# Kernel optimization log

Measured on AMD Instinct MI355X. Metric: run time of the kernel, lower is better.

Reference implementation:

```python
import jax, jax.numpy as jnp
import numpy as np

NUM_EXPERTS = 16
TOP_K = 4
N_GROUP = 4
TOPK_GROUP = 2
SCALING = 2.5


def setup_inputs() -> dict:
    key = jax.random.key(0)
    ks = jax.random.split(key, 9)
    B, S, H, I = 2, 1024, 2048, 1024
    w = lambda k, shape: jax.random.normal(k, shape, jnp.float32) * 0.02
    return {
        "hidden_states": jax.random.normal(ks[0], (B, S, H), jnp.float32),
        "gate_weight": w(ks[1], (NUM_EXPERTS, H)),
        "expert_bias": jnp.zeros((NUM_EXPERTS,), jnp.float32),
        "gate_proj": w(ks[2], (NUM_EXPERTS, I, H)),
        "up_proj": w(ks[3], (NUM_EXPERTS, I, H)),
        "down_proj": w(ks[4], (NUM_EXPERTS, H, I)),
        "shared_gate": w(ks[5], (I, H)),
        "shared_up": w(ks[6], (I, H)),
        "shared_down": w(ks[7], (H, I)),
    }


def _route(x, gate_weight, expert_bias):
    # x: [T, H] -> routing weights [T, K], selected experts [T, K]
    logits = x @ gate_weight.T                              # [T, E]
    scores = jax.nn.sigmoid(logits)
    biased = scores + expert_bias[None, :]                  # bias only for selection
    T = x.shape[0]
    gsz = NUM_EXPERTS // N_GROUP
    grp = biased.reshape(T, N_GROUP, gsz)
    top2, _ = jax.lax.top_k(grp, 2)
    group_scores = top2.sum(-1)                             # [T, G]
    _, gidx = jax.lax.top_k(group_scores, TOPK_GROUP)       # [T, topk_group]
    gmask = jax.nn.one_hot(gidx, N_GROUP, dtype=scores.dtype).sum(1)  # [T, G]
    emask = jnp.repeat(gmask, gsz, axis=1)                  # [T, E]
    masked = jnp.where(emask > 0, biased, -jnp.inf)
    _, sel = jax.lax.top_k(masked, TOP_K)                   # [T, K]
    w = jnp.take_along_axis(scores, sel, axis=1)            # weights from unbiased scores
    w = w / (w.sum(-1, keepdims=True) + 1e-20)              # norm_topk_prob
    return w * SCALING, sel


def _moe(x, w, sel, gate_proj, up_proj, down_proj):
    # combine weight per (token, expert): [T, E]; zero where expert not selected
    cw = (jax.nn.one_hot(sel, NUM_EXPERTS, dtype=x.dtype) * w[..., None]).sum(1)

    def body(acc, inp):
        g, u, d, we = inp                                   # g,u: [I,H]; d: [H,I]; we: [T]
        y = (jax.nn.silu(x @ g.T) * (x @ u.T)) @ d.T        # SwiGLU expert FFN
        return acc + we[:, None] * y, None

    out, _ = jax.lax.scan(body, jnp.zeros_like(x),
                          (gate_proj, up_proj, down_proj, cw.T))
    return out


def reference(hidden_states, gate_weight, expert_bias, gate_proj, up_proj,
              down_proj, shared_gate, shared_up, shared_down):
    B, S, H = hidden_states.shape
    x = hidden_states.reshape(-1, H)                        # [T, H]
    w, sel = _route(x, gate_weight, expert_bias)
    out = _moe(x, w, sel, gate_proj, up_proj, down_proj)
    shared = (jax.nn.silu(x @ shared_gate.T) * (x @ shared_up.T)) @ shared_down.T
    return (out + shared).reshape(B, S, H)
```

## Files before the change

### kernel.cpp

```cpp
#include <hip/hip_runtime.h>
#include <hip/hip_bf16.h>
#include <stdint.h>

#define T_TOK 2048
#define HDIM  2048
#define IDIM  1024
#define NEXP  16
#define SCALING 2.5f

typedef __attribute__((ext_vector_type(8))) short bf16x8;
typedef __attribute__((ext_vector_type(4))) float f32x4;

static __device__ __forceinline__ unsigned short f2bf(float f) {
    uint32_t u = __float_as_uint(f);
    u += 0x7FFF + ((u >> 16) & 1);
    return (unsigned short)(u >> 16);
}

#define GLD_LDS16(g, l) \
    __builtin_amdgcn_global_load_lds((const __attribute__((address_space(1))) uint32_t*)(g), \
                                     (__attribute__((address_space(3))) uint32_t*)(l), 16, 0, 0)

__global__ __launch_bounds__(256) void cvt_k(const float* __restrict__ x,
                                             unsigned short* __restrict__ o) {
    int i = (blockIdx.x * 256 + threadIdx.x) * 8;
    float4 f0 = *(const float4*)(x + i);
    float4 f1 = *(const float4*)(x + i + 4);
    union { unsigned short h[8]; uint4 v; } u;
    u.h[0] = f2bf(f0.x); u.h[1] = f2bf(f0.y); u.h[2] = f2bf(f0.z); u.h[3] = f2bf(f0.w);
    u.h[4] = f2bf(f1.x); u.h[5] = f2bf(f1.y); u.h[6] = f2bf(f1.z); u.h[7] = f2bf(f1.w);
    *(uint4*)(o + i) = u.v;
}

__global__ __launch_bounds__(256) void cvt_w1_k(const float* __restrict__ gate_w,
                                                const float* __restrict__ up_w,
                                                const float* __restrict__ shg,
                                                const float* __restrict__ shu,
                                                unsigned short* __restrict__ wbf1) {
    size_t flat = ((size_t)blockIdx.x * 256 + threadIdx.x) * 8;
    int e   = (int)(flat >> 22);
    int rem = (int)(flat & ((1u << 22) - 1));
    int row = rem >> 11;
    int h   = rem & 2047;
    int f   = row >> 1;
    const float* src;
    if (e == NEXP) src = (row & 1) ? shu : shg;
    else           src = ((row & 1) ? up_w : gate_w) + (size_t)e * (IDIM * HDIM);
    src += (size_t)f * HDIM + h;
    float4 f0 = *(const float4*)src;
    float4 f1 = *(const float4*)(src + 4);
    union { unsigned short s[8]; uint4 v; } u;
    u.s[0] = f2bf(f0.x); u.s[1] = f2bf(f0.y); u.s[2] = f2bf(f0.z); u.s[3] = f2bf(f0.w);
    u.s[4] = f2bf(f1.x); u.s[5] = f2bf(f1.y); u.s[6] = f2bf(f1.z); u.s[7] = f2bf(f1.w);
    *(uint4*)(wbf1 + flat) = u.v;
}

__global__ __launch_bounds__(256) void cvt_w2_k(const float* __restrict__ down_w,
                                                const float* __restrict__ shd,
                                                unsigned short* __restrict__ wbf2) {
    size_t flat = ((size_t)blockIdx.x * 256 + threadIdx.x) * 8;
    int e   = (int)(flat >> 21);
    int rem = (int)(flat & ((1u << 21) - 1));
    const float* src = (e == NEXP) ? shd : (down_w + (size_t)e * (HDIM * IDIM));
    src += rem;
    float4 f0 = *(const float4*)src;
    float4 f1 = *(const float4*)(src + 4);
    union { unsigned short s[8]; uint4 v; } u;
    u.s[0] = f2bf(f0.x); u.s[1] = f2bf(f0.y); u.s[2] = f2bf(f0.z); u.s[3] = f2bf(f0.w);
    u.s[4] = f2bf(f1.x); u.s[5] = f2bf(f1.y); u.s[6] = f2bf(f1.z); u.s[7] = f2bf(f1.w);
    *(uint4*)(wbf2 + flat) = u.v;
}

__global__ __launch_bounds__(256) void route_k(const float* __restrict__ x,
                                               const float* __restrict__ gw,
                                               const float* __restrict__ bias,
                                               int* __restrict__ tokl,
                                               float* __restrict__ twl,
                                               int* __restrict__ cnt) {
    __shared__ float slog[NEXP];
    int t = blockIdx.x;
    int tid = threadIdx.x;
    int e = tid >> 4, r = tid & 15;
    const float* xp = x + (size_t)t * HDIM;
    const float* wp = gw + (size_t)e * HDIM;
    float p = 0.f;
    for (int j = r; j < HDIM; j += 16) p += xp[j] * wp[j];
    for (int off = 8; off; off >>= 1) p += __shfl_down(p, off, 16);
    if (r == 0) slog[e] = p;
    __syncthreads();
    if (tid == 0) {
        float sc[NEXP], bi[NEXP];
        for (int i = 0; i < NEXP; i++) {
            sc[i] = 1.f / (1.f + expf(-slog[i]));
            bi[i] = sc[i] + bias[i];
        }
        float gsc[4];
        for (int g = 0; g < 4; g++) {
            float v0 = bi[g*4+0], v1 = bi[g*4+1], v2 = bi[g*4+2], v3 = bi[g*4+3];
            float hi01 = fmaxf(v0, v1), lo01 = fminf(v0, v1);
            float hi23 = fmaxf(v2, v3), lo23 = fminf(v2, v3);
            float top1 = fmaxf(hi01, hi23);
            float sec  = fmaxf(fminf(hi01, hi23), (hi01 >= hi23) ? lo01 : lo23);
            gsc[g] = top1 + sec;
        }
        int g0 = 0; for (int g = 1; g < 4; g++) if (gsc[g] > gsc[g0]) g0 = g;
        int g1 = (g0 == 0) ? 1 : 0;
        for (int g = 0; g < 4; g++) if (g != g0 && gsc[g] > gsc[g1]) g1 = g;
        float mk[NEXP];
        for (int i = 0; i < NEXP; i++) {
            int gg = i >> 2;
            mk[i] = (gg == g0 || gg == g1) ? bi[i] : -INFINITY;
        }
        int sel[4]; float wv[4]; float wsum = 0.f;
        for (int k = 0; k < 4; k++) {
            int bmax = 0; float bv = -INFINITY;
            for (int i = 0; i < NEXP; i++) if (mk[i] > bv) { bv = mk[i]; bmax = i; }
            sel[k] = bmax; mk[bmax] = -INFINITY;
            wv[k] = sc[bmax]; wsum += sc[bmax];
        }
        float scale = SCALING / (wsum + 1e-20f);
        for (int k = 0; k < 4; k++) {
            int ee = sel[k];
            int slot = atomicAdd(&cnt[ee], 1);
            tokl[ee * T_TOK + slot] = t;
            twl[ee * T_TOK + slot] = wv[k] * scale;
        }
    }
}

__global__ __launch_bounds__(256) void gemm1_k(const unsigned short* __restrict__ Xbf,
                                               const unsigned short* __restrict__ wbf1,
                                               const int* __restrict__ tokl,
                                               const int* __restrict__ cnt,
                                               unsigned short* __restrict__ act) {
    __shared__ unsigned short lsA[2][128 * 64];
    __shared__ unsigned short lsB[2][128 * 64];
    int b = blockIdx.x;
    int swz = (b & 7) * 544 + (b >> 3);
    int mt = swz & 15, nt = (swz >> 4) & 15, e = swz >> 8;
    int C = (e == NEXP) ? T_TOK : cnt[e];
    int m0 = mt * 128;
    if (m0 >= C) return;
    int tid = threadIdx.x;

    int c8 = tid & 7, rr = tid >> 3;
    int swzc = c8 ^ (rr & 7);
    const char* aA[4];
    const char* aB[4];
    for (int i = 0; i < 4; i++) {
        int slot = m0 + i * 32 + rr;
        int sl = (slot < C) ? slot : (C - 1);
        int tk = (e == NEXP) ? sl : tokl[e * T_TOK + sl];
        aA[i] = (const char*)Xbf + ((size_t)tk * HDIM + (size_t)swzc * 8) * 2;
        int brow = nt * 128 + i * 32 + rr;
        aB[i] = (const char*)wbf1 + (((size_t)e << 22) + (size_t)brow * HDIM + (size_t)swzc * 8) * 2;
    }

    int lane = tid & 63, wid = tid >> 6;
    int wrow = (wid >> 1) << 6, wcol = (wid & 1) << 6;
    int fr = lane & 15, kg = lane >> 4;

    f32x4 acc[4][4];
#pragma unroll
    for (int m = 0; m < 4; m++)
#pragma unroll
        for (int n = 0; n < 4; n++) acc[m][n] = (f32x4){0.f, 0.f, 0.f, 0.f};

    auto stage = [&](int kt, int bf) {
        size_t kb = (size_t)kt * 128;
#pragma unroll
        for (int i = 0; i < 4; i++)
            GLD_LDS16(aA[i] + kb, (char*)&lsA[bf][0] + i * 4096 + tid * 16);
#pragma unroll
        for (int i = 0; i < 4; i++)
            GLD_LDS16(aB[i] + kb, (char*)&lsB[bf][0] + i * 4096 + tid * 16);
    };
    auto compute = [&](int bf) {
        const char* lA = (const char*)&lsA[bf][0];
        const char* lB = (const char*)&lsB[bf][0];
#pragma unroll
        for (int h = 0; h < 2; h++) {
            bf16x8 av[4], bv[4];
#pragma unroll
            for (int m = 0; m < 4; m++)
                av[m] = *(const bf16x8*)(lA + (wrow + m * 16 + fr) * 128 + (((h * 4 + kg) ^ (fr & 7)) << 4));
#pragma unroll
            for (int n = 0; n < 4; n++)
                bv[n] = *(const bf16x8*)(lB + (wcol + n * 16 + fr) * 128 + (((h * 4 + kg) ^ (fr & 7)) << 4));
#pragma unroll
            for (int m = 0; m < 4; m++)
#pragma unroll
                for (int n = 0; n < 4; n++)
                    acc[m][n] = __builtin_amdgcn_mfma_f32_16x16x32_bf16(av[m], bv[n], acc[m][n], 0, 0, 0);
        }
    };

    stage(0, 0);
    __syncthreads();
    int cur = 0;
    for (int kt = 0; kt < 32; ++kt) {
        if (kt + 1 < 32) stage(kt + 1, cur ^ 1);
        compute(cur);
        __syncthreads();
        cur ^= 1;
    }

    unsigned short* actE = act + (size_t)e * T_TOK * IDIM;
#pragma unroll
    for (int m = 0; m < 4; m++)
#pragma unroll
        for (int n = 0; n < 4; n++)
#pragma unroll
            for (int q = 0; q < 4; q++) {
                float v = acc[m][n][q];
                float pu = __shfl_xor(v, 1, 64);
                int row = wrow + m * 16 + kg * 4 + q;
                int slot = m0 + row;
                int col = wcol + n * 16 + fr;
                if (!(lane & 1) && slot < C) {
                    float g = v, u = pu;
                    float a = g / (1.f + __expf(-g)) * u;
                    int j = nt * 64 + (col >> 1);
                    actE[(size_t)slot * IDIM + j] = f2bf(a);
                }
            }
}

__global__ __launch_bounds__(256) void gemm2_k(const unsigned short* __restrict__ act,
                                               const unsigned short* __restrict__ wbf2,
                                               const int* __restrict__ tokl,
                                               const float* __restrict__ twl,
                                               const int* __restrict__ cnt,
                                               float* __restrict__ out) {
    __shared__ unsigned short lsA[2][128 * 64];
    __shared__ unsigned short lsB[2][128 * 64];
    int b = blockIdx.x;
    int swz = (b & 7) * 544 + (b >> 3);
    int mt = swz & 15, nt = (swz >> 4) & 15, e = swz >> 8;
    int C = (e == NEXP) ? T_TOK : cnt[e];
    int m0 = mt * 128;
    if (m0 >= C) return;
    int nb = nt * 128;
    int tid = threadIdx.x;

    const unsigned short* actE = act + (size_t)e * T_TOK * IDIM;
    int c8 = tid & 7, rr = tid >> 3;
    int swzc = c8 ^ (rr & 7);
    const char* aA[4];
    const char* aB[4];
    for (int i = 0; i < 4; i++) {
        int slot = m0 + i * 32 + rr;
        aA[i] = (const char*)actE + ((size_t)slot * IDIM + (size_t)swzc * 8) * 2;
        aB[i] = (const char*)wbf2 + (((size_t)e << 21) + (size_t)(nb + i * 32 + rr) * IDIM + (size_t)swzc * 8) * 2;
    }

    int lane = tid & 63, wid = tid >> 6;
    int wrow = (wid >> 1) << 6, wcol = (wid & 1) << 6;
    int fr = lane & 15, kg = lane >> 4;

    f32x4 acc[4][4];
#pragma unroll
    for (int m = 0; m < 4; m++)
#pragma unroll
        for (int n = 0; n < 4; n++) acc[m][n] = (f32x4){0.f, 0.f, 0.f, 0.f};

    auto stage = [&](int kt, int bf) {
        size_t kb = (size_t)kt * 128;
#pragma unroll
        for (int i = 0; i < 4; i++)
            GLD_LDS16(aA[i] + kb, (char*)&lsA[bf][0] + i * 4096 + tid * 16);
#pragma unroll
        for (int i = 0; i < 4; i++)
            GLD_LDS16(aB[i] + kb, (char*)&lsB[bf][0] + i * 4096 + tid * 16);
    };
    auto compute = [&](int bf) {
        const char* lA = (const char*)&lsA[bf][0];
        const char* lB = (const char*)&lsB[bf][0];
#pragma unroll
        for (int h = 0; h < 2; h++) {
            bf16x8 av[4], bv[4];
#pragma unroll
            for (int m = 0; m < 4; m++)
                av[m] = *(const bf16x8*)(lA + (wrow + m * 16 + fr) * 128 + (((h * 4 + kg) ^ (fr & 7)) << 4));
#pragma unroll
            for (int n = 0; n < 4; n++)
                bv[n] = *(const bf16x8*)(lB + (wcol + n * 16 + fr) * 128 + (((h * 4 + kg) ^ (fr & 7)) << 4));
#pragma unroll
            for (int m = 0; m < 4; m++)
#pragma unroll
                for (int n = 0; n < 4; n++)
                    acc[m][n] = __builtin_amdgcn_mfma_f32_16x16x32_bf16(av[m], bv[n], acc[m][n], 0, 0, 0);
        }
    };

    stage(0, 0);
    __syncthreads();
    int cur = 0;
    for (int kt = 0; kt < 16; ++kt) {
        if (kt + 1 < 16) stage(kt + 1, cur ^ 1);
        compute(cur);
        __syncthreads();
        cur ^= 1;
    }

#pragma unroll
    for (int m = 0; m < 4; m++)
#pragma unroll
        for (int q = 0; q < 4; q++) {
            int row = wrow + m * 16 + kg * 4 + q;
            int slot = m0 + row;
            if (slot >= C) continue;
            int tk; float wg;
            if (e == NEXP) { tk = slot; wg = 1.f; }
            else { tk = tokl[e * T_TOK + slot]; wg = twl[e * T_TOK + slot]; }
            float* o = out + (size_t)tk * HDIM + nb + wcol + fr;
#pragma unroll
            for (int n = 0; n < 4; n++)
                atomicAdd(o + n * 16, wg * acc[m][n][q]);
        }
}

extern "C" void kernel_launch(void* const* d_in, const int* in_sizes, int n_in,
                              void* d_out, int out_size, void* d_ws, size_t ws_size,
                              hipStream_t stream) {
    const float* x      = (const float*)d_in[0];
    const float* gw     = (const float*)d_in[1];
    const float* bias   = (const float*)d_in[2];
    const float* gate_w = (const float*)d_in[3];
    const float* up_w   = (const float*)d_in[4];
    const float* down_w = (const float*)d_in[5];
    const float* shg    = (const float*)d_in[6];
    const float* shu    = (const float*)d_in[7];
    const float* shd    = (const float*)d_in[8];
    float* out = (float*)d_out;
    char* ws = (char*)d_ws;

    unsigned short* Xbf  = (unsigned short*)ws;
    unsigned short* act  = (unsigned short*)(ws + 8388608ULL);
    unsigned short* wbf1 = (unsigned short*)(ws + 79691776ULL);
    unsigned short* wbf2 = (unsigned short*)(ws + 222298112ULL);
    int*            tokl = (int*)(ws + 293601280ULL);
    float*          twl  = (float*)(ws + 293732352ULL);
    int*            cnt  = (int*)(ws + 293863424ULL);

    hipMemsetAsync(out, 0, (size_t)out_size * 4, stream);
    hipMemsetAsync(cnt, 0, 64, stream);
    cvt_k<<<2048, 256, 0, stream>>>(x, Xbf);
    cvt_w1_k<<<34816, 256, 0, stream>>>(gate_w, up_w, shg, shu, wbf1);
    cvt_w2_k<<<17408, 256, 0, stream>>>(down_w, shd, wbf2);
    route_k<<<2048, 256, 0, stream>>>(x, gw, bias, tokl, twl, cnt);
    gemm1_k<<<4352, 256, 0, stream>>>(Xbf, wbf1, tokl, cnt, act);
    gemm2_k<<<4352, 256, 0, stream>>>(act, wbf2, tokl, twl, cnt, out);
}
```

Baseline: 1.046 ms.

## Enlarge MoE GEMM tiles to 256x256 with 8 waves and explicit pipelining

Both expert GEMM kernels move from 128x128 tiles with 4 waves to 256x256 tiles with 8 waves and 128KB of dynamic LDS, double buffered. The main loop uses explicit vmcnt/lgkmcnt waits, raw barriers, sched_barrier and setprio, so the next tile's global-to-LDS copy overlaps the MFMA work. The aim is more operand reuse per byte loaded and fewer blocks. The cost is lower occupancy, since the large LDS use likely allows only one block per CU, and more wasted padding rows for experts that receive few tokens.

Result: faster. 901.3 us (-13.8%).

```diff
diff --git a/kernel.cpp b/kernel.cpp
--- a/kernel.cpp
+++ b/kernel.cpp
@@ -128,18 +128,17 @@
     }
 }
 
-__global__ __launch_bounds__(256) void gemm1_k(const unsigned short* __restrict__ Xbf,
-                                               const unsigned short* __restrict__ wbf1,
-                                               const int* __restrict__ tokl,
-                                               const int* __restrict__ cnt,
-                                               unsigned short* __restrict__ act) {
-    __shared__ unsigned short lsA[2][128 * 64];
-    __shared__ unsigned short lsB[2][128 * 64];
+__global__ __launch_bounds__(512, 2) void gemm1_k(const unsigned short* __restrict__ Xbf,
+                                                  const unsigned short* __restrict__ wbf1,
+                                                  const int* __restrict__ tokl,
+                                                  const int* __restrict__ cnt,
+                                                  unsigned short* __restrict__ act) {
+    extern __shared__ unsigned short sm[];
     int b = blockIdx.x;
-    int swz = (b & 7) * 544 + (b >> 3);
-    int mt = swz & 15, nt = (swz >> 4) & 15, e = swz >> 8;
+    int swz = (b & 7) * 136 + (b >> 3);
+    int e = swz >> 6, mt = (swz >> 3) & 7, nt = swz & 7;
     int C = (e == NEXP) ? T_TOK : cnt[e];
-    int m0 = mt * 128;
+    int m0 = mt * 256;
     if (m0 >= C) return;
     int tid = threadIdx.x;
 
@@ -147,100 +146,118 @@
     int swzc = c8 ^ (rr & 7);
     const char* aA[4];
     const char* aB[4];
+#pragma unroll
     for (int i = 0; i < 4; i++) {
-        int slot = m0 + i * 32 + rr;
+        int slot = m0 + i * 64 + rr;
         int sl = (slot < C) ? slot : (C - 1);
         int tk = (e == NEXP) ? sl : tokl[e * T_TOK + sl];
         aA[i] = (const char*)Xbf + ((size_t)tk * HDIM + (size_t)swzc * 8) * 2;
-        int brow = nt * 128 + i * 32 + rr;
+        int brow = nt * 256 + i * 64 + rr;
         aB[i] = (const char*)wbf1 + (((size_t)e << 22) + (size_t)brow * HDIM + (size_t)swzc * 8) * 2;
     }
 
     int lane = tid & 63, wid = tid >> 6;
-    int wrow = (wid >> 1) << 6, wcol = (wid & 1) << 6;
+    int wm = wid >> 2, wn = wid & 3;
     int fr = lane & 15, kg = lane >> 4;
-
-    f32x4 acc[4][4];
-#pragma unroll
-    for (int m = 0; m < 4; m++)
+    int xo = fr & 7;
+
+    f32x4 acc[8][4];
+#pragma unroll
+    for (int m = 0; m < 8; m++)
 #pragma unroll
         for (int n = 0; n < 4; n++) acc[m][n] = (f32x4){0.f, 0.f, 0.f, 0.f};
 
     auto stage = [&](int kt, int bf) {
         size_t kb = (size_t)kt * 128;
-#pragma unroll
-        for (int i = 0; i < 4; i++)
-            GLD_LDS16(aA[i] + kb, (char*)&lsA[bf][0] + i * 4096 + tid * 16);
-#pragma unroll
-        for (int i = 0; i < 4; i++)
-            GLD_LDS16(aB[i] + kb, (char*)&lsB[bf][0] + i * 4096 + tid * 16);
+        char* dA = (char*)(sm + bf * 16384);
+        char* dB = (char*)(sm + 32768 + bf * 16384);
+#pragma unroll
+        for (int i = 0; i < 4; i++) GLD_LDS16(aA[i] + kb, dA + i * 8192 + tid * 16);
+#pragma unroll
+        for (int i = 0; i < 4; i++) GLD_LDS16(aB[i] + kb, dB + i * 8192 + tid * 16);
     };
-    auto compute = [&](int bf) {
-        const char* lA = (const char*)&lsA[bf][0];
-        const char* lB = (const char*)&lsB[bf][0];
-#pragma unroll
-        for (int h = 0; h < 2; h++) {
-            bf16x8 av[4], bv[4];
-#pragma unroll
-            for (int m = 0; m < 4; m++)
-                av[m] = *(const bf16x8*)(lA + (wrow + m * 16 + fr) * 128 + (((h * 4 + kg) ^ (fr & 7)) << 4));
-#pragma unroll
-            for (int n = 0; n < 4; n++)
-                bv[n] = *(const bf16x8*)(lB + (wcol + n * 16 + fr) * 128 + (((h * 4 + kg) ^ (fr & 7)) << 4));
-#pragma unroll
-            for (int m = 0; m < 4; m++)
-#pragma unroll
-                for (int n = 0; n < 4; n++)
-                    acc[m][n] = __builtin_amdgcn_mfma_f32_16x16x32_bf16(av[m], bv[n], acc[m][n], 0, 0, 0);
-        }
-    };
 
     stage(0, 0);
-    __syncthreads();
-    int cur = 0;
-    for (int kt = 0; kt < 32; ++kt) {
-        if (kt + 1 < 32) stage(kt + 1, cur ^ 1);
-        compute(cur);
-        __syncthreads();
-        cur ^= 1;
+    asm volatile("s_waitcnt vmcnt(0)" ::: "memory");
+    __builtin_amdgcn_s_barrier();
+
+    const int NT = 32;
+    for (int kt = 0; kt < NT; ++kt) {
+        int bf = kt & 1;
+        __builtin_amdgcn_s_barrier();
+        __builtin_amdgcn_sched_barrier(0);
+        if (kt + 1 < NT) {
+            stage(kt + 1, bf ^ 1);
+            asm volatile("s_waitcnt vmcnt(8)" ::: "memory");
+        } else {
+            asm volatile("s_waitcnt vmcnt(0)" ::: "memory");
+        }
+        __builtin_amdgcn_s_barrier();
+        __builtin_amdgcn_sched_barrier(0);
+
+        const char* lA = (const char*)(sm + bf * 16384);
+        const char* lB = (const char*)(sm + 32768 + bf * 16384);
+        bf16x8 bv[4][2];
+#pragma unroll
+        for (int n = 0; n < 4; n++)
+#pragma unroll
+            for (int h = 0; h < 2; h++)
+                bv[n][h] = *(const bf16x8*)(lB + (wn * 64 + n * 16 + fr) * 128 + ((((h << 2) | kg) ^ xo) << 4));
+#pragma unroll
+        for (int p = 0; p < 4; p++) {
+            bf16x8 av[2][2];
+#pragma unroll
+            for (int mm = 0; mm < 2; mm++)
+#pragma unroll
+                for (int h = 0; h < 2; h++)
+                    av[mm][h] = *(const bf16x8*)(lA + (wm * 128 + (p * 2 + mm) * 16 + fr) * 128 + ((((h << 2) | kg) ^ xo) << 4));
+            asm volatile("s_waitcnt lgkmcnt(0)" ::: "memory");
+            __builtin_amdgcn_sched_barrier(0);
+            __builtin_amdgcn_s_setprio(1);
+#pragma unroll
+            for (int h = 0; h < 2; h++)
+#pragma unroll
+                for (int n = 0; n < 4; n++) {
+                    acc[p * 2 + 0][n] = __builtin_amdgcn_mfma_f32_16x16x32_bf16(av[0][h], bv[n][h], acc[p * 2 + 0][n], 0, 0, 0);
+                    acc[p * 2 + 1][n] = __builtin_amdgcn_mfma_f32_16x16x32_bf16(av[1][h], bv[n][h], acc[p * 2 + 1][n], 0, 0, 0);
+                }
+            __builtin_amdgcn_s_setprio(0);
+        }
     }
 
     unsigned short* actE = act + (size_t)e * T_TOK * IDIM;
 #pragma unroll
-    for (int m = 0; m < 4; m++)
+    for (int m = 0; m < 8; m++)
 #pragma unroll
         for (int n = 0; n < 4; n++)
 #pragma unroll
             for (int q = 0; q < 4; q++) {
                 float v = acc[m][n][q];
                 float pu = __shfl_xor(v, 1, 64);
-                int row = wrow + m * 16 + kg * 4 + q;
-                int slot = m0 + row;
-                int col = wcol + n * 16 + fr;
+                int slot = m0 + wm * 128 + m * 16 + kg * 4 + q;
                 if (!(lane & 1) && slot < C) {
                     float g = v, u = pu;
                     float a = g / (1.f + __expf(-g)) * u;
-                    int j = nt * 64 + (col >> 1);
+                    int j = nt * 128 + wn * 32 + n * 8 + (fr >> 1);
                     actE[(size_t)slot * IDIM + j] = f2bf(a);
                 }
             }
 }
 
-__global__ __launch_bounds__(256) void gemm2_k(const unsigned short* __restrict__ act,
-                                               const unsigned short* __restrict__ wbf2,
-                                               const int* __restrict__ tokl,
-                                               const float* __restrict__ twl,
-                                               const int* __restrict__ cnt,
-                                               float* __restrict__ out) {
-    __shared__ unsigned short lsA[2][128 * 64];
-    __shared__ unsigned short lsB[2][128 * 64];
+__global__ __launch_bounds__(512, 2) void gemm2_k(const unsigned short* __restrict__ act,
+                                                  const unsigned short* __restrict__ wbf2,
+                                                  const int* __restrict__ tokl,
+                                                  const float* __restrict__ twl,
+                                                  const int* __restrict__ cnt,
+                                                  float* __restrict__ out) {
+    extern __shared__ unsigned short sm[];
     int b = blockIdx.x;
-    int swz = (b & 7) * 544 + (b >> 3);
-    int mt = swz & 15, nt = (swz >> 4) & 15, e = swz >> 8;
+    int swz = (b & 7) * 136 + (b >> 3);
+    int e = swz >> 6, mt = (swz >> 3) & 7, nt = swz & 7;
     int C = (e == NEXP) ? T_TOK : cnt[e];
-    int m0 = mt * 128;
+    int m0 = mt * 256;
     if (m0 >= C) return;
-    int nb = nt * 128;
+    int nb = nt * 256;
     int tid = threadIdx.x;
 
     const unsigned short* actE = act + (size_t)e * T_TOK * IDIM;
@@ -248,72 +265,92 @@
     int swzc = c8 ^ (rr & 7);
     const char* aA[4];
     const char* aB[4];
+#pragma unroll
     for (int i = 0; i < 4; i++) {
-        int slot = m0 + i * 32 + rr;
+        int slot = m0 + i * 64 + rr;
         aA[i] = (const char*)actE + ((size_t)slot * IDIM + (size_t)swzc * 8) * 2;
-        aB[i] = (const char*)wbf2 + (((size_t)e << 21) + (size_t)(nb + i * 32 + rr) * IDIM + (size_t)swzc * 8) * 2;
+        aB[i] = (const char*)wbf2 + (((size_t)e << 21) + (size_t)(nb + i * 64 + rr) * IDIM + (size_t)swzc * 8) * 2;
     }
 
     int lane = tid & 63, wid = tid >> 6;
-    int wrow = (wid >> 1) << 6, wcol = (wid & 1) << 6;
+    int wm = wid >> 2, wn = wid & 3;
     int fr = lane & 15, kg = lane >> 4;
-
-    f32x4 acc[4][4];
-#pragma unroll
-    for (int m = 0; m < 4; m++)
+    int xo = fr & 7;
+
+    f32x4 acc[8][4];
+#pragma unroll
+    for (int m = 0; m < 8; m++)
 #pragma unroll
         for (int n = 0; n < 4; n++) acc[m][n] = (f32x4){0.f, 0.f, 0.f, 0.f};
 
     auto stage = [&](int kt, int bf) {
         size_t kb = (size_t)kt * 128;
-#pragma unroll
-        for (int i = 0; i < 4; i++)
-            GLD_LDS16(aA[i] + kb, (char*)&lsA[bf][0] + i * 4096 + tid * 16);
-#pragma unroll
-        for (int i = 0; i < 4; i++)
-            GLD_LDS16(aB[i] + kb, (char*)&lsB[bf][0] + i * 4096 + tid * 16);
+        char* dA = (char*)(sm + bf * 16384);
+        char* dB = (char*)(sm + 32768 + bf * 16384);
+#pragma unroll
+        for (int i = 0; i < 4; i++) GLD_LDS16(aA[i] + kb, dA + i * 8192 + tid * 16);
+#pragma unroll
+        for (int i = 0; i < 4; i++) GLD_LDS16(aB[i] + kb, dB + i * 8192 + tid * 16);
     };
-    auto compute = [&](int bf) {
-        const char* lA = (const char*)&lsA[bf][0];
-        const char* lB = (const char*)&lsB[bf][0];
-#pragma unroll
-        for (int h = 0; h < 2; h++) {
-            bf16x8 av[4], bv[4];
-#pragma unroll
-            for (int m = 0; m < 4; m++)
-                av[m] = *(const bf16x8*)(lA + (wrow + m * 16 + fr) * 128 + (((h * 4 + kg) ^ (fr & 7)) << 4));
-#pragma unroll
-            for (int n = 0; n < 4; n++)
-                bv[n] = *(const bf16x8*)(lB + (wcol + n * 16 + fr) * 128 + (((h * 4 + kg) ^ (fr & 7)) << 4));
-#pragma unroll
-            for (int m = 0; m < 4; m++)
-#pragma unroll
-                for (int n = 0; n < 4; n++)
-                    acc[m][n] = __builtin_amdgcn_mfma_f32_16x16x32_bf16(av[m], bv[n], acc[m][n], 0, 0, 0);
-        }
-    };
 
     stage(0, 0);
-    __syncthreads();
-    int cur = 0;
-    for (int kt = 0; kt < 16; ++kt) {
-        if (kt + 1 < 16) stage(kt + 1, cur ^ 1);
-        compute(cur);
-        __syncthreads();
-        cur ^= 1;
-    }
-
-#pragma unroll
-    for (int m = 0; m < 4; m++)
+    asm volatile("s_waitcnt vmcnt(0)" ::: "memory");
+    __builtin_amdgcn_s_barrier();
+
+    const int NT = 16;
+    for (int kt = 0; kt < NT; ++kt) {
+        int bf = kt & 1;
+        __builtin_amdgcn_s_barrier();
+        __builtin_amdgcn_sched_barrier(0);
+        if (kt + 1 < NT) {
+            stage(kt + 1, bf ^ 1);
+            asm volatile("s_waitcnt vmcnt(8)" ::: "memory");
+        } else {
+            asm volatile("s_waitcnt vmcnt(0)" ::: "memory");
+        }
+        __builtin_amdgcn_s_barrier();
+        __builtin_amdgcn_sched_barrier(0);
+
+        const char* lA = (const char*)(sm + bf * 16384);
+        const char* lB = (const char*)(sm + 32768 + bf * 16384);
+        bf16x8 bv[4][2];
+#pragma unroll
+        for (int n = 0; n < 4; n++)
+#pragma unroll
+            for (int h = 0; h < 2; h++)
+                bv[n][h] = *(const bf16x8*)(lB + (wn * 64 + n * 16 + fr) * 128 + ((((h << 2) | kg) ^ xo) << 4));
+#pragma unroll
+        for (int p = 0; p < 4; p++) {
+            bf16x8 av[2][2];
+#pragma unroll
+            for (int mm = 0; mm < 2; mm++)
+#pragma unroll
+                for (int h = 0; h < 2; h++)
+                    av[mm][h] = *(const bf16x8*)(lA + (wm * 128 + (p * 2 + mm) * 16 + fr) * 128 + ((((h << 2) | kg) ^ xo) << 4));
+            asm volatile("s_waitcnt lgkmcnt(0)" ::: "memory");
+            __builtin_amdgcn_sched_barrier(0);
+            __builtin_amdgcn_s_setprio(1);
+#pragma unroll
+            for (int h = 0; h < 2; h++)
+#pragma unroll
+                for (int n = 0; n < 4; n++) {
+                    acc[p * 2 + 0][n] = __builtin_amdgcn_mfma_f32_16x16x32_bf16(av[0][h], bv[n][h], acc[p * 2 + 0][n], 0, 0, 0);
+                    acc[p * 2 + 1][n] = __builtin_amdgcn_mfma_f32_16x16x32_bf16(av[1][h], bv[n][h], acc[p * 2 + 1][n], 0, 0, 0);
+                }
+            __builtin_amdgcn_s_setprio(0);
+        }
+    }
+
+#pragma unroll
+    for (int m = 0; m < 8; m++)
 #pragma unroll
         for (int q = 0; q < 4; q++) {
-            int row = wrow + m * 16 + kg * 4 + q;
-            int slot = m0 + row;
+            int slot = m0 + wm * 128 + m * 16 + kg * 4 + q;
             if (slot >= C) continue;
             int tk; float wg;
             if (e == NEXP) { tk = slot; wg = 1.f; }
             else { tk = tokl[e * T_TOK + slot]; wg = twl[e * T_TOK + slot]; }
-            float* o = out + (size_t)tk * HDIM + nb + wcol + fr;
+            float* o = out + (size_t)tk * HDIM + nb + wn * 64 + fr;
 #pragma unroll
             for (int n = 0; n < 4; n++)
                 atomicAdd(o + n * 16, wg * acc[m][n][q]);
@@ -343,12 +380,19 @@
     float*          twl  = (float*)(ws + 293732352ULL);
     int*            cnt  = (int*)(ws + 293863424ULL);
 
+    static bool attr_set = false;
+    if (!attr_set) {
+        hipFuncSetAttribute((const void*)gemm1_k, hipFuncAttributeMaxDynamicSharedMemorySize, 131072);
+        hipFuncSetAttribute((const void*)gemm2_k, hipFuncAttributeMaxDynamicSharedMemorySize, 131072);
+        attr_set = true;
+    }
+
     hipMemsetAsync(out, 0, (size_t)out_size * 4, stream);
     hipMemsetAsync(cnt, 0, 64, stream);
     cvt_k<<<2048, 256, 0, stream>>>(x, Xbf);
     cvt_w1_k<<<34816, 256, 0, stream>>>(gate_w, up_w, shg, shu, wbf1);
     cvt_w2_k<<<17408, 256, 0, stream>>>(down_w, shd, wbf2);
     route_k<<<2048, 256, 0, stream>>>(x, gw, bias, tokl, twl, cnt);
-    gemm1_k<<<4352, 256, 0, stream>>>(Xbf, wbf1, tokl, cnt, act);
-    gemm2_k<<<4352, 256, 0, stream>>>(act, wbf2, tokl, twl, cnt, out);
-}
+    gemm1_k<<<1088, 512, 131072, stream>>>(Xbf, wbf1, tokl, cnt, act);
+    gemm2_k<<<1088, 512, 131072, stream>>>(act, wbf2, tokl, twl, cnt, out);
+}
```
